# Optimization experiments

Measured on AMD Instinct MI355X. Metric: run time of the kernel, lower is better.

The kernel has to match this reference:

```python
import jax, jax.numpy as jnp
import numpy as np

N_NODES = 100000
N_EDGES = 1600000
NUM_GRAPHS = 1024
D_IN = 128
D_HID = 128
D_OUT = 2
LN_EPS = 1e-5


def setup_inputs() -> dict:
    key = jax.random.key(0)
    ks = jax.random.split(key, 10)
    x = jax.random.normal(ks[0], (N_NODES, D_IN), dtype=jnp.float32)
    edge_index = jax.random.randint(ks[1], (2, N_EDGES), 0, N_NODES, dtype=jnp.int64)
    batch = jnp.sort(jax.random.randint(ks[2], (N_NODES,), 0, NUM_GRAPHS, dtype=jnp.int64))
    s = 0.05  # weight scale to keep activations sane
    return {
        "x": x,
        "edge_index": edge_index,
        "batch": batch,
        "W1l": jax.random.normal(ks[3], (D_HID, D_IN), dtype=jnp.float32) * s,
        "b1l": jnp.zeros((D_HID,), dtype=jnp.float32),
        "W1r": jax.random.normal(ks[4], (D_HID, D_IN), dtype=jnp.float32) * s,
        "W2l": jax.random.normal(ks[5], (D_HID, D_HID), dtype=jnp.float32) * s,
        "b2l": jnp.zeros((D_HID,), dtype=jnp.float32),
        "W2r": jax.random.normal(ks[6], (D_HID, D_HID), dtype=jnp.float32) * s,
        "ln_g": jnp.ones((D_HID,), dtype=jnp.float32),
        "ln_b": jnp.zeros((D_HID,), dtype=jnp.float32),
        "Wlin": jax.random.normal(ks[7], (D_OUT, D_HID), dtype=jnp.float32) * s,
        "blin": jnp.zeros((D_OUT,), dtype=jnp.float32),
    }


def _sage_conv(x, src, dst, Wl, bl, Wr):
    # PyG SAGEConv with mean aggregation: lin_l(mean_{j in N(i)} x_j) + lin_r(x_i)
    msg_sum = jax.ops.segment_sum(x[src], dst, num_segments=N_NODES)
    deg = jax.ops.segment_sum(jnp.ones((src.shape[0], 1), x.dtype), dst, num_segments=N_NODES)
    agg = msg_sum / jnp.maximum(deg, 1.0)  # isolated nodes -> 0
    return agg @ Wl.T + bl + x @ Wr.T  # lin_r has no bias (PyG default)


def reference(x, edge_index, batch, W1l, b1l, W1r, W2l, b2l, W2r, ln_g, ln_b, Wlin, blin):
    src, dst = edge_index[0], edge_index[1]
    h = jax.nn.relu(_sage_conv(x, src, dst, W1l, b1l, W1r))
    h = jax.nn.relu(_sage_conv(h, src, dst, W2l, b2l, W2r))
    # global_add_pool over graphs
    g = jax.ops.segment_sum(h, batch, num_segments=NUM_GRAPHS)  # [G, D_HID]
    # LayerNorm over last dim
    mu = jnp.mean(g, axis=-1, keepdims=True)
    var = jnp.var(g, axis=-1, keepdims=True)
    gn = (g - mu) * jax.lax.rsqrt(var + LN_EPS) * ln_g + ln_b
    return gn @ Wlin.T + blin  # [G, D_OUT]
```

## Files before the change

kernel.cpp:

```cpp
#include <hip/hip_runtime.h>
#include <hip/hip_bf16.h>
#include <hip/hip_fp8.h>

#define N_NODES   100000
#define N_EDGES   1600000
#define NUM_GRAPHS 1024
#define D         128
#define LN_EPS    1e-5f
#define NBUCKETS  391
#define CAP       4864
#define CHUNK     4096

typedef __attribute__((ext_vector_type(8))) short short8;
typedef __attribute__((ext_vector_type(4))) float floatx4;
typedef __attribute__((ext_vector_type(2))) float f32x2;

static __device__ __forceinline__ float bf2f(unsigned int u) {
    return __uint_as_float(u << 16);
}
static __device__ __forceinline__ unsigned short f2bf(float f) {
    __hip_bfloat16 h = __float2bfloat16(f);
    return *reinterpret_cast<unsigned short*>(&h);
}
static __device__ __forceinline__ void acc4(f32x2* acc, uint4 v) {
    acc[0] += (f32x2){__uint_as_float(v.x << 16), __uint_as_float(v.x & 0xffff0000u)};
    acc[1] += (f32x2){__uint_as_float(v.y << 16), __uint_as_float(v.y & 0xffff0000u)};
    acc[2] += (f32x2){__uint_as_float(v.z << 16), __uint_as_float(v.z & 0xffff0000u)};
    acc[3] += (f32x2){__uint_as_float(v.w << 16), __uint_as_float(v.w & 0xffff0000u)};
}

#if __has_builtin(__builtin_amdgcn_cvt_pk_f32_fp8)
#define UNPK_FP8(x, w) __builtin_amdgcn_cvt_pk_f32_fp8((x), (w))
#else
static __device__ __forceinline__ f32x2 unpk_fp8_sw(unsigned x, bool w) {
    unsigned s = w ? (x >> 16) : (x & 0xffffu);
    __hip_fp8_e4m3 a, b;
    *reinterpret_cast<unsigned char*>(&a) = (unsigned char)(s & 0xff);
    *reinterpret_cast<unsigned char*>(&b) = (unsigned char)((s >> 8) & 0xff);
    return (f32x2){(float)a, (float)b};
}
#define UNPK_FP8(x, w) unpk_fp8_sw((x), (w))
#endif

#if __has_builtin(__builtin_amdgcn_cvt_pk_fp8_f32)
#define PK_FP8(a, b, old, w) ((unsigned)__builtin_amdgcn_cvt_pk_fp8_f32((a), (b), (int)(old), (w)))
#else
static __device__ __forceinline__ unsigned pk_fp8_sw(float a, float b) {
    __hip_fp8_e4m3 fa = (__hip_fp8_e4m3)a;
    __hip_fp8_e4m3 fb = (__hip_fp8_e4m3)b;
    return (unsigned)*reinterpret_cast<unsigned char*>(&fa) |
           ((unsigned)*reinterpret_cast<unsigned char*>(&fb) << 8);
}
#define PK_FP8(a, b, old, w) ((w) ? ((((unsigned)(old)) & 0xffffu) | (pk_fp8_sw((a),(b)) << 16)) \
                                  : ((((unsigned)(old)) & 0xffff0000u) | pk_fp8_sw((a),(b))))
#endif

static __device__ __forceinline__ unsigned char fp8b(float v) {
    __hip_fp8_e4m3 t = (__hip_fp8_e4m3)v;
    return *reinterpret_cast<unsigned char*>(&t);
}

__global__ __launch_bounds__(256)
void prep_kernel(const float* __restrict__ x, unsigned short* __restrict__ xbf,
                 unsigned* __restrict__ xf8,
                 const float* __restrict__ W1l, const float* __restrict__ W1r,
                 const float* __restrict__ W2l, const float* __restrict__ W2r,
                 unsigned short* __restrict__ Wc1, unsigned short* __restrict__ Wc2,
                 int* __restrict__ cursor) {
    int i = blockIdx.x * 256 + threadIdx.x;
    float4 v = reinterpret_cast<const float4*>(x)[i];
    ushort4 o;
    o.x = f2bf(v.x); o.y = f2bf(v.y); o.z = f2bf(v.z); o.w = f2bf(v.w);
    reinterpret_cast<ushort4*>(xbf)[i] = o;
    unsigned p = PK_FP8(v.x, v.y, 0u, false);
    p = PK_FP8(v.z, v.w, p, true);
    xf8[i] = p;
    if (blockIdx.x < 256) {
        int layer = i >> 15;
        int rem = i & 32767;
        int c = rem >> 8;
        int k = rem & 255;
        const float* Wl = layer ? W2l : W1l;
        const float* Wr = layer ? W2r : W1r;
        unsigned short* dst = layer ? Wc2 : Wc1;
        float wv = (k < 128) ? Wl[c * 128 + k] : Wr[c * 128 + (k - 128)];
        dst[c * 256 + k] = f2bf(wv);
    }
    if (blockIdx.x == 256) {
        for (int b = threadIdx.x; b < NBUCKETS; b += 256)
            cursor[b] = b * CAP;
        if (threadIdx.x < 32)
            xf8[(size_t)N_NODES * 32 + threadIdx.x] = 0u;
    }
}

__global__ __launch_bounds__(256)
void bin_scatter_kernel(const int* __restrict__ src, const int* __restrict__ dst,
                        int* __restrict__ cursor, unsigned* __restrict__ binned) {
    __shared__ int cnt[NBUCKETS];
    __shared__ int base[NBUCKETS];
    int chunkBase = blockIdx.x * CHUNK;
    for (int i = threadIdx.x; i < NBUCKETS; i += 256) cnt[i] = 0;
    __syncthreads();
    int es[16], ed[16], lofs[16];
    #pragma unroll
    for (int j = 0; j < 16; ++j) {
        int e = chunkBase + j * 256 + threadIdx.x;
        if (e < N_EDGES) {
            es[j] = src[e];
            ed[j] = dst[e];
            lofs[j] = atomicAdd(&cnt[ed[j] >> 8], 1);
        }
    }
    __syncthreads();
    for (int i = threadIdx.x; i < NBUCKETS; i += 256) {
        int c = cnt[i];
        base[i] = c ? atomicAdd(&cursor[i], c) : 0;
    }
    __syncthreads();
    #pragma unroll
    for (int j = 0; j < 16; ++j) {
        int e = chunkBase + j * 256 + threadIdx.x;
        if (e < N_EDGES) {
            int b = ed[j] >> 8;
            int pos = base[b] + lofs[j];
            if (pos < (b + 1) * CAP)
                binned[pos] = ((unsigned)(ed[j] & 255) << 17) | (unsigned)es[j];
        }
    }
}

__global__ __launch_bounds__(256)
void bucket_build_kernel(const unsigned* __restrict__ binned, const int* __restrict__ cursor,
                         int2* __restrict__ row_info, int* __restrict__ src_sorted) {
    __shared__ int scnt[256];
    __shared__ int sscan[256];
    int b = blockIdx.x;
    int t = threadIdx.x;
    int lo = b * CAP;
    int hi = cursor[b];
    int cap_end = lo + CAP;
    if (hi > cap_end) hi = cap_end;
    scnt[t] = 0;
    __syncthreads();
    unsigned rec[19];
    short rnk[19];
    #pragma unroll
    for (int i = 0; i < 19; ++i) {
        int e = lo + t + i * 256;
        if (e < hi) {
            unsigned r = binned[e];
            rec[i] = r;
            rnk[i] = (short)atomicAdd(&scnt[r >> 17], 1);
        }
    }
    __syncthreads();
    int v = scnt[t];
    sscan[t] = v;
    __syncthreads();
    for (int off = 1; off < 256; off <<= 1) {
        int a = (t >= off) ? sscan[t - off] : 0;
        __syncthreads();
        sscan[t] += a;
        __syncthreads();
    }
    int ex = sscan[t] - v;
    int node = b * 256 + t;
    if (node < N_NODES) row_info[node] = make_int2(lo + ex, v);
    scnt[t] = ex;
    __syncthreads();
    #pragma unroll
    for (int i = 0; i < 19; ++i) {
        int e = lo + t + i * 256;
        if (e < hi) {
            unsigned r = rec[i];
            src_sorted[lo + scnt[r >> 17] + rnk[i]] = (int)(r & 0x1FFFFu);
        }
    }
}

__global__ __launch_bounds__(256)
void aggregate_kernel(const unsigned char* __restrict__ feat8,
                      const int* __restrict__ src_sorted,
                      const int2* __restrict__ row_info,
                      unsigned short* __restrict__ aggout) {
    int tid  = threadIdx.x;
    int wave = tid >> 6;
    int lane = tid & 63;
    int l16  = lane & 15;
    int grpbase = lane & 48;
    int node = blockIdx.x * 16 + wave * 4 + (lane >> 4);
    int2 ri = row_info[node];
    int s = ri.x, deg = ri.y;
    int dmax = deg;
    dmax = max(dmax, __shfl_xor(dmax, 16, 64));
    dmax = max(dmax, __shfl_xor(dmax, 32, 64));
    unsigned chb = (unsigned)l16 * 8;
    f32x2 a0[4], a1[4];
    #pragma unroll
    for (int i = 0; i < 4; ++i) { a0[i] = (f32x2){0.f, 0.f}; a1[i] = (f32x2){0.f, 0.f}; }

    for (int c0 = 0; c0 < dmax; c0 += 16) {
        int si = src_sorted[s + c0 + l16];
        int rel = deg - c0;
        int rend = dmax - c0; if (rend > 16) rend = 16;
        int r = 0;
        for (; r + 2 <= rend; r += 2) {
            int u0 = __shfl(si, grpbase + r, 64);
            int u1 = __shfl(si, grpbase + r + 1, 64);
            u0 = (r < rel) ? u0 : N_NODES;
            u1 = (r + 1 < rel) ? u1 : N_NODES;
            uint2 v0 = *(const uint2*)(feat8 + (((unsigned)u0 << 7) + chb));
            uint2 v1 = *(const uint2*)(feat8 + (((unsigned)u1 << 7) + chb));
            a0[0] += UNPK_FP8(v0.x, false);
            a0[1] += UNPK_FP8(v0.x, true);
            a0[2] += UNPK_FP8(v0.y, false);
            a0[3] += UNPK_FP8(v0.y, true);
            a1[0] += UNPK_FP8(v1.x, false);
            a1[1] += UNPK_FP8(v1.x, true);
            a1[2] += UNPK_FP8(v1.y, false);
            a1[3] += UNPK_FP8(v1.y, true);
        }
        if (r < rend) {
            int u0 = __shfl(si, grpbase + r, 64);
            u0 = (r < rel) ? u0 : N_NODES;
            uint2 v0 = *(const uint2*)(feat8 + (((unsigned)u0 << 7) + chb));
            a0[0] += UNPK_FP8(v0.x, false);
            a0[1] += UNPK_FP8(v0.x, true);
            a0[2] += UNPK_FP8(v0.y, false);
            a0[3] += UNPK_FP8(v0.y, true);
        }
    }
    float inv = 1.f / (float)(deg > 1 ? deg : 1);
    f32x2 t0 = (a0[0] + a1[0]) * inv;
    f32x2 t1 = (a0[1] + a1[1]) * inv;
    f32x2 t2 = (a0[2] + a1[2]) * inv;
    f32x2 t3 = (a0[3] + a1[3]) * inv;
    uint4 o;
    o.x = (unsigned)f2bf(t0.x) | ((unsigned)f2bf(t0.y) << 16);
    o.y = (unsigned)f2bf(t1.x) | ((unsigned)f2bf(t1.y) << 16);
    o.z = (unsigned)f2bf(t2.x) | ((unsigned)f2bf(t2.y) << 16);
    o.w = (unsigned)f2bf(t3.x) | ((unsigned)f2bf(t3.y) << 16);
    *(uint4*)(aggout + (size_t)node * 128 + l16 * 8) = o;
}

__global__ __launch_bounds__(256)
void gemm_kernel(const unsigned short* __restrict__ A1,
                 const unsigned short* __restrict__ A2,
                 const unsigned short* __restrict__ Wcat,
                 const float* __restrict__ bias,
                 unsigned short* __restrict__ out,
                 unsigned char* __restrict__ f8out) {
    int tid = threadIdx.x;
    int wave = tid >> 6;
    int lane = tid & 63;
    int quad = lane >> 4, m = lane & 15;
    int nodeBase = blockIdx.x * 64;

    short8 bw[2][8];
    #pragma unroll
    for (int cb = 0; cb < 2; ++cb) {
        const unsigned short* wp = Wcat + (size_t)(wave * 32 + cb * 16 + m) * 256 + quad * 8;
        #pragma unroll
        for (int kc = 0; kc < 8; ++kc)
            bw[cb][kc] = *(const short8*)(wp + kc * 32);
    }

    floatx4 acc[4][2];
    #pragma unroll
    for (int a = 0; a < 4; ++a)
        #pragma unroll
        for (int b = 0; b < 2; ++b) acc[a][b] = (floatx4){0.f, 0.f, 0.f, 0.f};

    #pragma unroll
    for (int kc = 0; kc < 8; ++kc) {
        const unsigned short* Asrc = (kc < 4) ? A1 : A2;
        int kOff = (kc & 3) * 32;
        const unsigned short* ap = Asrc + (size_t)(nodeBase + m) * 128 + kOff + quad * 8;
        short8 afr[4];
        #pragma unroll
        for (int nb = 0; nb < 4; ++nb)
            afr[nb] = *(const short8*)(ap + (size_t)nb * 16 * 128);
        #pragma unroll
        for (int nb = 0; nb < 4; ++nb)
            #pragma unroll
            for (int cb = 0; cb < 2; ++cb)
                acc[nb][cb] = __builtin_amdgcn_mfma_f32_16x16x32_bf16(afr[nb], bw[cb][kc], acc[nb][cb], 0, 0, 0);
    }

    #pragma unroll
    for (int cb = 0; cb < 2; ++cb) {
        int col = wave * 32 + cb * 16 + m;
        float bv = bias[col];
        #pragma unroll
        for (int nb = 0; nb < 4; ++nb) {
            #pragma unroll
            for (int rr = 0; rr < 4; ++rr) {
                int row = nodeBase + nb * 16 + quad * 4 + rr;
                if (row < N_NODES) {
                    float v = acc[nb][cb][rr] + bv;
                    v = v > 0.f ? v : 0.f;
                    out[(size_t)row * 128 + col] = f2bf(v);
                    if (f8out) f8out[(size_t)row * 128 + col] = fp8b(v);
                }
            }
        }
    }
}

__global__ __launch_bounds__(256)
void pool_ln_out_kernel(const unsigned short* __restrict__ h2,
                        const int* __restrict__ batch,
                        const float* __restrict__ ln_g, const float* __restrict__ ln_b,
                        const float* __restrict__ Wlin, const float* __restrict__ blin,
                        float* __restrict__ out) {
    int g = blockIdx.x;
    int t = threadIdx.x;
    int lane = t & 63, w = t >> 6;
    __shared__ int se[2];
    if (t < 2) {
        int target = g + t;
        int lo = 0, hi = N_NODES;
        while (lo < hi) {
            int mid = (lo + hi) >> 1;
            if (batch[mid] < target) lo = mid + 1; else hi = mid;
        }
        se[t] = lo;
    }
    __syncthreads();
    int s = se[0], e = se[1];
    int ns = t >> 4;
    int chg = t & 15;
    f32x2 a[4];
    a[0] = a[1] = a[2] = a[3] = (f32x2){0.f, 0.f};
    for (int n = s + ns; n < e; n += 16) {
        uint4 v = *(const uint4*)(h2 + (size_t)n * 128 + chg * 8);
        acc4(a, v);
    }
    #pragma unroll
    for (int i = 0; i < 4; ++i) {
        a[i].x += __shfl_xor(a[i].x, 16, 64);
        a[i].y += __shfl_xor(a[i].y, 16, 64);
        a[i].x += __shfl_xor(a[i].x, 32, 64);
        a[i].y += __shfl_xor(a[i].y, 32, 64);
    }
    __shared__ float sw[4][128];
    if (lane < 16) {
        #pragma unroll
        for (int k = 0; k < 4; ++k) {
            sw[w][chg * 8 + 2 * k]     = a[k].x;
            sw[w][chg * 8 + 2 * k + 1] = a[k].y;
        }
    }
    __syncthreads();
    __shared__ float red[128];
    float sum = 0.f;
    if (t < 128) {
        sum = sw[0][t] + sw[1][t] + sw[2][t] + sw[3][t];
        red[t] = sum;
    }
    __syncthreads();
    for (int off = 64; off > 0; off >>= 1) {
        if (t < off) red[t] += red[t + off];
        __syncthreads();
    }
    float mu = red[0] * (1.f / 128.f);
    __syncthreads();
    float dv = sum - mu;
    if (t < 128) red[t] = dv * dv;
    __syncthreads();
    for (int off = 64; off > 0; off >>= 1) {
        if (t < off) red[t] += red[t + off];
        __syncthreads();
    }
    float var = red[0] * (1.f / 128.f);
    __syncthreads();
    __shared__ float r0[128], r1[128];
    if (t < 128) {
        float gn = dv * rsqrtf(var + LN_EPS) * ln_g[t] + ln_b[t];
        r0[t] = gn * Wlin[t];
        r1[t] = gn * Wlin[128 + t];
    }
    __syncthreads();
    for (int off = 64; off > 0; off >>= 1) {
        if (t < off) { r0[t] += r0[t + off]; r1[t] += r1[t + off]; }
        __syncthreads();
    }
    if (t == 0) {
        out[g * 2 + 0] = r0[0] + blin[0];
        out[g * 2 + 1] = r1[0] + blin[1];
    }
}

extern "C" void kernel_launch(void* const* d_in, const int* in_sizes, int n_in,
                              void* d_out, int out_size, void* d_ws, size_t ws_size,
                              hipStream_t stream) {
    const float* x    = (const float*)d_in[0];
    const int*   ei   = (const int*)d_in[1];
    const int*   batch= (const int*)d_in[2];
    const float* W1l  = (const float*)d_in[3];
    const float* b1l  = (const float*)d_in[4];
    const float* W1r  = (const float*)d_in[5];
    const float* W2l  = (const float*)d_in[6];
    const float* b2l  = (const float*)d_in[7];
    const float* W2r  = (const float*)d_in[8];
    const float* ln_g = (const float*)d_in[9];
    const float* ln_b = (const float*)d_in[10];
    const float* Wlin = (const float*)d_in[11];
    const float* blin = (const float*)d_in[12];
    float* out = (float*)d_out;

    char* ws = (char*)d_ws;
    size_t off = 0;
    auto alloc = [&](size_t bytes) {
        char* p = ws + off;
        off = (off + bytes + 255) & ~(size_t)255;
        return p;
    };
    unsigned short* xbf  = (unsigned short*)alloc((size_t)N_NODES * D * 2);
    unsigned short* aggb = (unsigned short*)alloc((size_t)N_NODES * D * 2);
    unsigned short* h1   = (unsigned short*)alloc((size_t)N_NODES * D * 2);
    unsigned*       xf8  = (unsigned*)alloc((size_t)N_NODES * D + 128);
    unsigned short* Wc1  = (unsigned short*)alloc(128 * 256 * 2);
    unsigned short* Wc2  = (unsigned short*)alloc(128 * 256 * 2);
    int2* row_info   = (int2*)alloc((size_t)N_NODES * 8);
    int* src_sorted  = (int*)alloc(((size_t)NBUCKETS * CAP + 8192) * 4);
    int* cursor      = (int*)alloc(NBUCKETS * 4);
    unsigned* binned = (unsigned*)aggb;
    unsigned char* h1f8 = (unsigned char*)xf8;

    const int* srcI = ei;
    const int* dstI = ei + N_EDGES;

    prep_kernel<<<12500, 256, 0, stream>>>(x, xbf, xf8, W1l, W1r, W2l, W2r, Wc1, Wc2, cursor);
    bin_scatter_kernel<<<(N_EDGES + CHUNK - 1) / CHUNK, 256, 0, stream>>>(srcI, dstI, cursor, binned);
    bucket_build_kernel<<<NBUCKETS, 256, 0, stream>>>(binned, cursor, row_info, src_sorted);

    aggregate_kernel<<<6250, 256, 0, stream>>>((const unsigned char*)xf8, src_sorted, row_info, aggb);
    gemm_kernel<<<1563, 256, 0, stream>>>(aggb, xbf, Wc1, b1l, h1, h1f8);
    aggregate_kernel<<<6250, 256, 0, stream>>>(h1f8, src_sorted, row_info, aggb);
    gemm_kernel<<<1563, 256, 0, stream>>>(aggb, h1, Wc2, b2l, xbf, nullptr);
    pool_ln_out_kernel<<<NUM_GRAPHS, 256, 0, stream>>>(xbf, batch, ln_g, ln_b, Wlin, blin, out);
}
```

Baseline: 335.0 us.

## Stage GEMM weights in swizzled LDS, double node tile, split FP8 conversion

```diff
diff --git a/kernel.cpp b/kernel.cpp
--- a/kernel.cpp
+++ b/kernel.cpp
@@ -54,11 +54,6 @@
 #define PK_FP8(a, b, old, w) ((w) ? ((((unsigned)(old)) & 0xffffu) | (pk_fp8_sw((a),(b)) << 16)) \
                                   : ((((unsigned)(old)) & 0xffff0000u) | pk_fp8_sw((a),(b))))
 #endif
-
-static __device__ __forceinline__ unsigned char fp8b(float v) {
-    __hip_fp8_e4m3 t = (__hip_fp8_e4m3)v;
-    return *reinterpret_cast<unsigned char*>(&t);
-}
 
 __global__ __launch_bounds__(256)
 void prep_kernel(const float* __restrict__ x, unsigned short* __restrict__ xbf,
@@ -95,6 +90,21 @@
 }
 
 __global__ __launch_bounds__(256)
+void cvt_h1_kernel(const unsigned short* __restrict__ h1, uint2* __restrict__ h1f8) {
+    int i = blockIdx.x * 256 + threadIdx.x;
+    uint4 v = reinterpret_cast<const uint4*>(h1)[i];
+    float c0 = __uint_as_float(v.x << 16), c1 = __uint_as_float(v.x & 0xffff0000u);
+    float c2 = __uint_as_float(v.y << 16), c3 = __uint_as_float(v.y & 0xffff0000u);
+    float c4 = __uint_as_float(v.z << 16), c5 = __uint_as_float(v.z & 0xffff0000u);
+    float c6 = __uint_as_float(v.w << 16), c7 = __uint_as_float(v.w & 0xffff0000u);
+    unsigned lo = PK_FP8(c0, c1, 0u, false);
+    lo = PK_FP8(c2, c3, lo, true);
+    unsigned hi = PK_FP8(c4, c5, 0u, false);
+    hi = PK_FP8(c6, c7, hi, true);
+    h1f8[i] = make_uint2(lo, hi);
+}
+
+__global__ __launch_bounds__(256)
 void bin_scatter_kernel(const int* __restrict__ src, const int* __restrict__ dst,
                         int* __restrict__ cursor, unsigned* __restrict__ binned) {
     __shared__ int cnt[NBUCKETS];
@@ -244,48 +254,64 @@
     *(uint4*)(aggout + (size_t)node * 128 + l16 * 8) = o;
 }
 
+static __device__ __forceinline__ int wswz(int kq, int col) {
+    return kq * 128 + (col ^ ((kq & 3) | (((col >> 3) & 1) << 2)));
+}
+
 __global__ __launch_bounds__(256)
 void gemm_kernel(const unsigned short* __restrict__ A1,
                  const unsigned short* __restrict__ A2,
                  const unsigned short* __restrict__ Wcat,
                  const float* __restrict__ bias,
-                 unsigned short* __restrict__ out,
-                 unsigned char* __restrict__ f8out) {
+                 unsigned short* __restrict__ out) {
+    __shared__ unsigned short Wsm[32 * 128 * 8];
     int tid = threadIdx.x;
     int wave = tid >> 6;
     int lane = tid & 63;
     int quad = lane >> 4, m = lane & 15;
-    int nodeBase = blockIdx.x * 64;
-
-    short8 bw[2][8];
-    #pragma unroll
-    for (int cb = 0; cb < 2; ++cb) {
-        const unsigned short* wp = Wcat + (size_t)(wave * 32 + cb * 16 + m) * 256 + quad * 8;
-        #pragma unroll
-        for (int kc = 0; kc < 8; ++kc)
-            bw[cb][kc] = *(const short8*)(wp + kc * 32);
-    }
-
-    floatx4 acc[4][2];
-    #pragma unroll
-    for (int a = 0; a < 4; ++a)
+    int nodeBase = blockIdx.x * 128;
+
+    #pragma unroll
+    for (int j = 0; j < 16; ++j) {
+        int c = tid + j * 256;
+        int kq = c >> 7, col = c & 127;
+        *(uint4*)(&Wsm[wswz(kq, col) * 8]) =
+            *(const uint4*)(Wcat + col * 256 + kq * 8);
+    }
+
+    int rofs[8];
+    #pragma unroll
+    for (int nb = 0; nb < 8; ++nb) {
+        int rA = nodeBase + nb * 16 + m;
+        if (rA > N_NODES - 1) rA = N_NODES - 1;
+        rofs[nb] = rA * 128;
+    }
+
+    floatx4 acc[8][2];
+    #pragma unroll
+    for (int a = 0; a < 8; ++a)
         #pragma unroll
         for (int b = 0; b < 2; ++b) acc[a][b] = (floatx4){0.f, 0.f, 0.f, 0.f};
+
+    __syncthreads();
 
     #pragma unroll
     for (int kc = 0; kc < 8; ++kc) {
         const unsigned short* Asrc = (kc < 4) ? A1 : A2;
-        int kOff = (kc & 3) * 32;
-        const unsigned short* ap = Asrc + (size_t)(nodeBase + m) * 128 + kOff + quad * 8;
-        short8 afr[4];
-        #pragma unroll
-        for (int nb = 0; nb < 4; ++nb)
-            afr[nb] = *(const short8*)(ap + (size_t)nb * 16 * 128);
-        #pragma unroll
-        for (int nb = 0; nb < 4; ++nb)
+        int kOff = (kc & 3) * 32 + quad * 8;
+        short8 afr[8];
+        #pragma unroll
+        for (int nb = 0; nb < 8; ++nb)
+            afr[nb] = *(const short8*)(Asrc + rofs[nb] + kOff);
+        short8 bfr[2];
+        #pragma unroll
+        for (int cb = 0; cb < 2; ++cb)
+            bfr[cb] = *(const short8*)(&Wsm[wswz(kc * 4 + quad, wave * 32 + cb * 16 + m) * 8]);
+        #pragma unroll
+        for (int nb = 0; nb < 8; ++nb)
             #pragma unroll
             for (int cb = 0; cb < 2; ++cb)
-                acc[nb][cb] = __builtin_amdgcn_mfma_f32_16x16x32_bf16(afr[nb], bw[cb][kc], acc[nb][cb], 0, 0, 0);
+                acc[nb][cb] = __builtin_amdgcn_mfma_f32_16x16x32_bf16(afr[nb], bfr[cb], acc[nb][cb], 0, 0, 0);
     }
 
     #pragma unroll
@@ -293,7 +319,7 @@
         int col = wave * 32 + cb * 16 + m;
         float bv = bias[col];
         #pragma unroll
-        for (int nb = 0; nb < 4; ++nb) {
+        for (int nb = 0; nb < 8; ++nb) {
             #pragma unroll
             for (int rr = 0; rr < 4; ++rr) {
                 int row = nodeBase + nb * 16 + quad * 4 + rr;
@@ -301,7 +327,6 @@
                     float v = acc[nb][cb][rr] + bv;
                     v = v > 0.f ? v : 0.f;
                     out[(size_t)row * 128 + col] = f2bf(v);
-                    if (f8out) f8out[(size_t)row * 128 + col] = fp8b(v);
                 }
             }
         }
@@ -427,7 +452,7 @@
     int* src_sorted  = (int*)alloc(((size_t)NBUCKETS * CAP + 8192) * 4);
     int* cursor      = (int*)alloc(NBUCKETS * 4);
     unsigned* binned = (unsigned*)aggb;
-    unsigned char* h1f8 = (unsigned char*)xf8;
+    uint2* h1f8      = (uint2*)xf8;
 
     const int* srcI = ei;
     const int* dstI = ei + N_EDGES;
@@ -437,8 +462,9 @@
     bucket_build_kernel<<<NBUCKETS, 256, 0, stream>>>(binned, cursor, row_info, src_sorted);
 
     aggregate_kernel<<<6250, 256, 0, stream>>>((const unsigned char*)xf8, src_sorted, row_info, aggb);
-    gemm_kernel<<<1563, 256, 0, stream>>>(aggb, xbf, Wc1, b1l, h1, h1f8);
-    aggregate_kernel<<<6250, 256, 0, stream>>>(h1f8, src_sorted, row_info, aggb);
-    gemm_kernel<<<1563, 256, 0, stream>>>(aggb, h1, Wc2, b2l, xbf, nullptr);
+    gemm_kernel<<<782, 256, 0, stream>>>(aggb, xbf, Wc1, b1l, h1);
+    cvt_h1_kernel<<<6250, 256, 0, stream>>>(h1, h1f8);
+    aggregate_kernel<<<6250, 256, 0, stream>>>((const unsigned char*)h1f8, src_sorted, row_info, aggb);
+    gemm_kernel<<<782, 256, 0, stream>>>(aggb, h1, Wc2, b2l, xbf);
     pool_ln_out_kernel<<<NUM_GRAPHS, 256, 0, stream>>>(xbf, batch, ln_g, ln_b, Wlin, blin, out);
 }
```

Result: slower. 349.1 us (+4.2%).
